# Performance work log

Measured on AMD Instinct MI355X. Metric: run time of the kernel, lower is better.

## Reference

```python
import jax, jax.numpy as jnp
import numpy as np

B, S, D, O, E = 8, 4096, 1024, 1024, 64

def setup_inputs() -> dict:
    key = jax.random.key(0)
    kx, kgw, kgb, kew, keb = jax.random.split(key, 5)
    x = jax.random.normal(kx, (B, S, D), dtype=jnp.float32)
    gate_w = jax.random.normal(kgw, (E, D), dtype=jnp.float32) * 0.02
    gate_b = jnp.zeros((E,), dtype=jnp.float32)
    expert_w = jax.random.normal(kew, (E, D, O), dtype=jnp.float32) * 0.02
    expert_b = jnp.zeros((E, O), dtype=jnp.float32)
    return {"x": x, "gate_w": gate_w, "gate_b": gate_b,
            "expert_w": expert_w, "expert_b": expert_b}

def reference(x, gate_w, gate_b, expert_w, expert_b):
    # x: [B,S,D] -> flatten tokens. With world_size=1 the all-reduce and
    # all-to-alls in the torch module are identities, and per-chunk processing
    # is token-independent, so one global pass is mathematically identical.
    b, s, d = x.shape
    xt = x.reshape(-1, d)                                   # [N, D]
    logits = xt @ gate_w.T + gate_b                         # [N, E]
    gates = jax.nn.softmax(logits, axis=-1)
    sel = jnp.argmax(gates, axis=-1)                        # [N] top-1 expert
    order = jnp.argsort(sel)                                # stable sort by expert
    xs = xt[order]                                          # tokens grouped by expert
    counts = jnp.bincount(sel, length=E).astype(jnp.int32)  # tokens per expert
    # Grouped expert GEMM: row block e of xs multiplies expert_w[e].
    ys = jax.lax.ragged_dot(xs, expert_w, counts)           # [N, O]
    ys = ys + expert_b[sel[order]]
    # Combine: scatter sorted outputs back to original token positions.
    # (Note: torch output is NOT scaled by gate probability.)
    out = jnp.zeros((xt.shape[0], expert_w.shape[-1]), dtype=ys.dtype)
    out = out.at[order].set(ys)
    return out.reshape(b, s, -1)
```

## Files before the change

### kernel.cpp

```cpp
#include <hip/hip_runtime.h>
#include <hip/hip_bf16.h>

#define N_TOK 32768
#define DIM 1024
#define OUTD 1024
#define NEXP 64

typedef __attribute__((ext_vector_type(4))) float f32x4;
typedef __attribute__((ext_vector_type(8))) short bf16x8;

__device__ __forceinline__ unsigned short f2bf(float f) {
    unsigned int u = __builtin_bit_cast(unsigned int, f);
    u += 0x7FFFu + ((u >> 16) & 1u);
    return (unsigned short)(u >> 16);
}

__device__ __forceinline__ uint4 pack8(float4 a, float4 b) {
    uint4 p;
    p.x = (unsigned int)f2bf(a.x) | ((unsigned int)f2bf(a.y) << 16);
    p.y = (unsigned int)f2bf(a.z) | ((unsigned int)f2bf(a.w) << 16);
    p.z = (unsigned int)f2bf(b.x) | ((unsigned int)f2bf(b.y) << 16);
    p.w = (unsigned int)f2bf(b.z) | ((unsigned int)f2bf(b.w) << 16);
    return p;
}

__device__ __forceinline__ float4 ntload4(const float* p) {
    f32x4 v = __builtin_nontemporal_load(reinterpret_cast<const f32x4*>(p));
    float4 r; r.x = v[0]; r.y = v[1]; r.z = v[2]; r.w = v[3];
    return r;
}

#define GLOAD16(gp, lp) \
    __builtin_amdgcn_global_load_lds((const __attribute__((address_space(1))) void*)(gp), \
                                     (__attribute__((address_space(3))) void*)(lp), 16, 0, 0)

__global__ __launch_bounds__(256) void prep_kernel(const float* __restrict__ x,
        const float* __restrict__ gw, const float* __restrict__ gb,
        const float* __restrict__ ew,
        int* __restrict__ sel, int* __restrict__ nflag, int* __restrict__ flags,
        int* __restrict__ counts,
        unsigned short* __restrict__ xb, unsigned short* __restrict__ wt)
{
    __shared__ __align__(16) char smem[18688];
    int tid = threadIdx.x;

    if (blockIdx.x < 512) {
        unsigned short* Ag = (unsigned short*)smem;
        unsigned short* Bg = (unsigned short*)(smem + 8192);
        int* h = (int*)(smem + 16384);
        if (tid < NEXP) h[tid] = 0;

        int t0 = blockIdx.x * 64;
        int lane = tid & 63;
        int w = tid >> 6;
        int lr = lane & 15, lg = lane >> 4;

        int rowS = tid >> 2;
        int koffS = (((tid & 3) ^ ((tid >> 3) & 3)) * 8);
        const float* xsrc = x + (size_t)(t0 + rowS) * DIM + koffS;
        const float* wsrc = gw + (size_t)rowS * DIM + koffS;
        unsigned short* xdst = xb ? xb + (size_t)(t0 + rowS) * DIM + koffS : nullptr;

        f32x4 acc[4];
#pragma unroll
        for (int n = 0; n < 4; n++)
#pragma unroll
            for (int c = 0; c < 4; c++) acc[n][c] = 0.f;

        float4 v0 = *reinterpret_cast<const float4*>(xsrc);
        float4 v1 = *reinterpret_cast<const float4*>(xsrc + 4);
        float4 v2 = *reinterpret_cast<const float4*>(wsrc);
        float4 v3 = *reinterpret_cast<const float4*>(wsrc + 4);
        {
            uint4 pa = pack8(v0, v1), pb = pack8(v2, v3);
            *reinterpret_cast<uint4*>(&Ag[tid * 8]) = pa;
            *reinterpret_cast<uint4*>(&Bg[tid * 8]) = pb;
            if (xdst) *reinterpret_cast<uint4*>(xdst) = pa;
        }
        __syncthreads();

        const char* Agc = (const char*)Ag;
        const char* Bgc = (const char*)Bg;
        int fko = (lg ^ ((lr >> 1) & 3)) * 16;

#pragma unroll 1
        for (int t = 0; t < 32; ++t) {
            if (t < 31) {
                int k0 = (t + 1) * 32;
                v0 = *reinterpret_cast<const float4*>(xsrc + k0);
                v1 = *reinterpret_cast<const float4*>(xsrc + k0 + 4);
                v2 = *reinterpret_cast<const float4*>(wsrc + k0);
                v3 = *reinterpret_cast<const float4*>(wsrc + k0 + 4);
            }
            int boff = (t & 1) * 4096;
            bf16x8 afr = *reinterpret_cast<const bf16x8*>(Agc + boff + ((w * 16 + lr) << 6) + fko);
#pragma unroll
            for (int n = 0; n < 4; n++) {
                bf16x8 bfr = *reinterpret_cast<const bf16x8*>(Bgc + boff + ((n * 16 + lr) << 6) + fko);
                acc[n] = __builtin_amdgcn_mfma_f32_16x16x32_bf16(afr, bfr, acc[n], 0, 0, 0);
            }
            if (t < 31) {
                uint4 pa = pack8(v0, v1), pb = pack8(v2, v3);
                int soff = ((t + 1) & 1) * 2048;
                *reinterpret_cast<uint4*>(&Ag[soff + tid * 8]) = pa;
                *reinterpret_cast<uint4*>(&Bg[soff + tid * 8]) = pb;
                if (xdst) *reinterpret_cast<uint4*>(xdst + (t + 1) * 32) = pa;
            }
            __syncthreads();
        }

        float gbv[4];
#pragma unroll
        for (int n = 0; n < 4; n++) gbv[n] = gb[n * 16 + lr];
#pragma unroll
        for (int i = 0; i < 4; i++) {
            float m1 = -1e30f, m2 = -1e30f; int e1 = 0;
#pragma unroll
            for (int n = 0; n < 4; n++) {
                float v = acc[n][i] + gbv[n];
                if (v > m1) { m2 = m1; m1 = v; e1 = n * 16 + lr; }
                else if (v > m2) m2 = v;
            }
#pragma unroll
            for (int d = 1; d < 16; d <<= 1) {
                float om1 = __shfl_xor(m1, d, 16);
                float om2 = __shfl_xor(m2, d, 16);
                int   oe1 = __shfl_xor(e1, d, 16);
                if (om1 > m1 || (om1 == m1 && oe1 < e1)) {
                    m2 = fmaxf(om2, m1); m1 = om1; e1 = oe1;
                } else {
                    m2 = fmaxf(m2, om1);
                }
            }
            if (lr == 0) {
                int t = t0 + w * 16 + lg * 4 + i;
                sel[t] = e1;
                atomicAdd(&h[e1], 1);
                if (m1 - m2 < 0.01f) {
                    int idx = atomicAdd(nflag, 1);
                    if (idx < 16384) flags[idx] = t;
                }
            }
        }
        __syncthreads();
        if (tid < NEXP && h[tid]) atomicAdd(&counts[tid], h[tid]);
    } else {
        if (!wt) return;
        unsigned short* ts0 = (unsigned short*)smem;
        unsigned short* ts1 = (unsigned short*)(smem + 9216);
        int lin = blockIdx.x - 512;
        int e = lin >> 5;
        int d0 = ((lin >> 4) & 1) * 512;
        int o0 = (lin & 15) * 64;
        const float* src = ew + (size_t)e * (DIM * OUTD);
        unsigned short* dst = wt + (size_t)e * (DIM * OUTD);
        int og = tid & 7;
        int dl = tid >> 3;
        int dc = tid & 7;
        int ol = tid >> 3;

        float4 c0, c1, c2, c3;
        {
            const float* sr0 = &src[(size_t)(d0 + dl) * OUTD + o0 + og * 8];
            const float* sr1 = &src[(size_t)(d0 + dl + 32) * OUTD + o0 + og * 8];
            c0 = ntload4(sr0);
            c1 = ntload4(sr0 + 4);
            c2 = ntload4(sr1);
            c3 = ntload4(sr1 + 4);
        }
#pragma unroll
        for (int s = 0; s < 8; ++s) {
            float4 n0 = c0, n1 = c1, n2 = c2, n3 = c3;
            if (s < 7) {
                int dsn = d0 + (s + 1) * 64;
                const float* sr0 = &src[(size_t)(dsn + dl) * OUTD + o0 + og * 8];
                const float* sr1 = &src[(size_t)(dsn + dl + 32) * OUTD + o0 + og * 8];
                n0 = ntload4(sr0);
                n1 = ntload4(sr0 + 4);
                n2 = ntload4(sr1);
                n3 = ntload4(sr1 + 4);
            }
            unsigned short* tsb = (s & 1) ? ts1 : ts0;
#pragma unroll
            for (int half = 0; half < 2; ++half) {
                int dLoc = dl + 32 * half;
                float4 va = half ? c2 : c0;
                float4 vb = half ? c3 : c1;
                unsigned short b[8] = { f2bf(va.x), f2bf(va.y), f2bf(va.z), f2bf(va.w),
                                        f2bf(vb.x), f2bf(vb.y), f2bf(vb.z), f2bf(vb.w) };
                int dg = dLoc >> 3, dr = dLoc & 7;
#pragma unroll
                for (int k = 0; k < 8; k++) {
                    int o = og * 8 + k;
                    int key = (o & 7) ^ ((o >> 3) & 7);
                    tsb[o * 72 + ((dg ^ key) << 3) + dr] = b[k];
                }
            }
            __syncthreads();
            int ds0 = d0 + s * 64;
#pragma unroll
            for (int i = 0; i < 2; i++) {
                int o = ol + 32 * i;
                int key = (o & 7) ^ ((o >> 3) & 7);
                uint4 v = *reinterpret_cast<const uint4*>(&tsb[o * 72 + ((dc ^ key) << 3)]);
                *reinterpret_cast<uint4*>(&dst[(size_t)(o0 + o) * DIM + ds0 + dc * 8]) = v;
            }
            c0 = n0; c1 = n1; c2 = n2; c3 = n3;
        }
    }
}

__global__ __launch_bounds__(256) void gate_fix_kernel(const float* __restrict__ x,
        const float* __restrict__ gw, const float* __restrict__ gb,
        int* __restrict__ sel, const int* __restrict__ nflag, const int* __restrict__ flags,
        int* __restrict__ counts)
{
    int n = *nflag; if (n > 16384) n = 16384;
    int fi = blockIdx.x * 4 + (threadIdx.x >> 6);
    if (fi >= n) return;
    int t = flags[fi];
    int e = threadIdx.x & 63;
    const float* xr = x + (size_t)t * DIM;
    const float* wr = gw + (size_t)e * DIM;
    double acc = (double)gb[e];
    for (int k = 0; k < DIM; k += 4) {
        acc += (double)xr[k]   * (double)wr[k];
        acc += (double)xr[k+1] * (double)wr[k+1];
        acc += (double)xr[k+2] * (double)wr[k+2];
        acc += (double)xr[k+3] * (double)wr[k+3];
    }
    double m1 = acc; int e1 = e;
#pragma unroll
    for (int d = 1; d < 64; d <<= 1) {
        double om1 = __shfl_xor(m1, d, 64);
        int   oe1  = __shfl_xor(e1, d, 64);
        if (om1 > m1 || (om1 == m1 && oe1 < e1)) { m1 = om1; e1 = oe1; }
    }
    if (e == 0) {
        int eOld = sel[t];
        if (eOld != e1) {
            sel[t] = e1;
            atomicSub(&counts[eOld], 1);
            atomicAdd(&counts[e1], 1);
        }
    }
}

__global__ void sched_kernel(const int* __restrict__ counts, int* __restrict__ offsets,
                             int* __restrict__ schedE, int* __restrict__ schedR,
                             int* __restrict__ totalRB, int rowsShift)
{
    int e = threadIdx.x;
    int c = counts[e];
    int v = c;
#pragma unroll
    for (int d = 1; d < 64; d <<= 1) { int y = __shfl_up(v, d, 64); if (e >= d) v += y; }
    offsets[e] = v - c;
    if (e == 63) offsets[NEXP] = v;
    int rows = 1 << rowsShift;
    int nb = (c + rows - 1) >> rowsShift;
    int rbv = nb;
#pragma unroll
    for (int d = 1; d < 64; d <<= 1) { int y = __shfl_up(rbv, d, 64); if (e >= d) rbv += y; }
    int rbBase = rbv - nb;
    for (int i = 0; i < nb; i++) { schedE[rbBase + i] = e; schedR[rbBase + i] = i << rowsShift; }
    if (e == 63) *totalRB = rbv;
}

__global__ __launch_bounds__(256) void scatter_kernel(const int* __restrict__ sel,
        const int* __restrict__ offsets, int* __restrict__ cursor, int* __restrict__ perm)
{
    int t = blockIdx.x * 256 + threadIdx.x;
    int e = sel[t];
    int pos = offsets[e] + atomicAdd(&cursor[e], 1);
    perm[pos] = t;
}

__global__ __launch_bounds__(512, 4) void moe_gemm7(
        const unsigned short* __restrict__ xb, const unsigned short* __restrict__ wt,
        const float* __restrict__ eb,
        const int* __restrict__ perm, const int* __restrict__ offsets,
        const int* __restrict__ counts, const int* __restrict__ schedE,
        const int* __restrict__ schedR, const int* __restrict__ totalRB,
        float* __restrict__ out)
{
    int idx = blockIdx.x;
    int xcd = idx & 7;
    int s = idx >> 3;
    int cb = s & 7;
    int rb = (s >> 3) * 8 + xcd;
    if (rb >= *totalRB) return;
    int e = schedE[rb], r0 = schedR[rb];
    int cnt = counts[e], base = offsets[e];

    __shared__ __align__(16) unsigned short As[24576];
    __shared__ __align__(16) unsigned short Bs[12288];

    int tid = threadIdx.x;
    int lane = tid & 63;
    int wv = tid >> 6;
    int wr = wv >> 1, wc = wv & 1;
    int lr = lane & 15, lg = lane >> 4;

    int rowS = tid >> 2;
    int koff = ((tid & 3) ^ ((tid >> 3) & 3)) * 8;
    int rA1 = r0 + rowS, rA2 = r0 + 128 + rowS;
    int tokA1 = (rA1 < cnt) ? perm[base + rA1] : 0;
    int tokA2 = (rA2 < cnt) ? perm[base + rA2] : 0;

    const unsigned short* wte = wt + ((size_t)e << 20);
    const unsigned short* aSrc1 = xb + (size_t)tokA1 * DIM + koff;
    const unsigned short* aSrc2 = xb + (size_t)tokA2 * DIM + koff;
    const unsigned short* bSrc1 = wte + (size_t)(cb * 128 + rowS) * DIM + koff;

    unsigned short* AsQ0 = As + wv * 512;
    unsigned short* AsQ1 = As + 4096 + wv * 512;
    unsigned short* BsQ0 = Bs + wv * 512;

    f32x4 acc[4][4];
#pragma unroll
    for (int m = 0; m < 4; m++)
#pragma unroll
        for (int n = 0; n < 4; n++)
#pragma unroll
            for (int c = 0; c < 4; c++) acc[m][n][c] = 0.f;

    const char* Asc = (const char*)As;
    const char* Bsc = (const char*)Bs;
    int fko = (lg ^ ((lr >> 1) & 3)) * 16;

    auto stage = [&](int buf, int k0) {
        GLOAD16(aSrc1 + k0, AsQ0 + buf * 8192);
        GLOAD16(aSrc2 + k0, AsQ1 + buf * 8192);
        GLOAD16(bSrc1 + k0, BsQ0 + buf * 4096);
    };
    auto compute = [&](int buf) {
        int aoff = buf * 16384;
        int boff = buf * 8192;
        bf16x8 bfr[4];
#pragma unroll
        for (int n = 0; n < 4; n++) {
            int row = wc * 64 + n * 16 + lr;
            bfr[n] = *reinterpret_cast<const bf16x8*>(Bsc + boff + (row << 6) + fko);
        }
        __builtin_amdgcn_s_setprio(1);
#pragma unroll
        for (int m = 0; m < 4; m++) {
            int row = wr * 64 + m * 16 + lr;
            bf16x8 afr = *reinterpret_cast<const bf16x8*>(Asc + aoff + (row << 6) + fko);
#pragma unroll
            for (int n = 0; n < 4; n++)
                acc[m][n] = __builtin_amdgcn_mfma_f32_16x16x32_bf16(afr, bfr[n], acc[m][n], 0, 0, 0);
        }
        __builtin_amdgcn_s_setprio(0);
    };

    stage(0, 0);
    stage(1, 32);

    int cbuf = 0, sbuf = 2;
#pragma unroll 1
    for (int t = 0; t < 30; ++t) {
        asm volatile("s_waitcnt vmcnt(3)" ::: "memory");
        __builtin_amdgcn_s_barrier();
        stage(sbuf, (t + 2) * 32);
        compute(cbuf);
        cbuf = (cbuf == 2) ? 0 : cbuf + 1;
        sbuf = (sbuf == 2) ? 0 : sbuf + 1;
    }
    asm volatile("s_waitcnt vmcnt(3)" ::: "memory");
    __builtin_amdgcn_s_barrier();
    compute(cbuf);
    cbuf = (cbuf == 2) ? 0 : cbuf + 1;
    asm volatile("s_waitcnt vmcnt(0)" ::: "memory");
    __builtin_amdgcn_s_barrier();
    compute(cbuf);

    float bias[4];
#pragma unroll
    for (int n = 0; n < 4; n++)
        bias[n] = eb[e * OUTD + cb * 128 + wc * 64 + n * 16 + lr];
#pragma unroll
    for (int m = 0; m < 4; m++) {
        int rowLoc = wr * 64 + m * 16 + lg * 4;
#pragma unroll
        for (int i2 = 0; i2 < 4; i2++) {
            int r = r0 + rowLoc + i2;
            if (r < cnt) {
                int tk = perm[base + r];
                float* op = out + (size_t)tk * OUTD + cb * 128 + wc * 64 + lr;
#pragma unroll
                for (int n = 0; n < 4; n++)
                    __builtin_nontemporal_store(acc[m][n][i2] + bias[n], op + n * 16);
            }
        }
    }
}

extern "C" void kernel_launch(void* const* d_in, const int* in_sizes, int n_in,
                              void* d_out, int out_size, void* d_ws, size_t ws_size,
                              hipStream_t stream)
{
    const float* x  = (const float*)d_in[0];
    const float* gw = (const float*)d_in[1];
    const float* gb = (const float*)d_in[2];
    const float* ew = (const float*)d_in[3];
    const float* eb = (const float*)d_in[4];
    float* out = (float*)d_out;

    char* ws = (char*)d_ws;
    int* counts  = (int*)(ws + 0);
    int* cursor  = (int*)(ws + 256);
    int* offsets = (int*)(ws + 512);
    int* totalRB = (int*)(ws + 1024);
    int* nflag   = (int*)(ws + 1028);
    int* schedE  = (int*)(ws + 2048);
    int* schedR  = (int*)(ws + 4096);
    int* flags   = (int*)(ws + 8192);
    int* sel     = (int*)(ws + 131072);
    int* perm    = (int*)(ws + 262144);

    const size_t WT_OFF   = (size_t)1 << 20;
    const size_t WT_BYTES = (size_t)NEXP * DIM * OUTD * 2;
    const size_t XB_OFF   = WT_OFF + WT_BYTES;
    const size_t XB_BYTES = (size_t)N_TOK * DIM * 2;
    int mode = (ws_size >= XB_OFF + XB_BYTES) ? 2 : 0;
    unsigned short* wt = (mode == 2) ? (unsigned short*)(ws + WT_OFF) : nullptr;
    unsigned short* xb = (mode == 2) ? (unsigned short*)(ws + XB_OFF) : nullptr;

    hipMemsetAsync(ws, 0, 2048, stream);

    prep_kernel<<<dim3(512 + ((mode == 2) ? 2048 : 0)), 256, 0, stream>>>(
        x, gw, gb, ew, sel, nflag, flags, counts, xb, wt);
    gate_fix_kernel<<<dim3(4096), 256, 0, stream>>>(x, gw, gb, sel, nflag, flags, counts);
    sched_kernel<<<dim3(1), 64, 0, stream>>>(counts, offsets, schedE, schedR, totalRB, 8);
    scatter_kernel<<<dim3(N_TOK / 256), 256, 0, stream>>>(sel, offsets, cursor, perm);

    moe_gemm7<<<dim3(1536), 512, 0, stream>>>(xb, wt, eb, perm, offsets, counts,
                                              schedE, schedR, totalRB, out);
}
```

Measured before the change: 379.2 us.

## Fuse gate fix, schedule and scatter into one last-block-ticket kernel

```diff
diff --git a/kernel.cpp b/kernel.cpp
--- a/kernel.cpp
+++ b/kernel.cpp
@@ -210,70 +210,91 @@
     }
 }
 
-__global__ __launch_bounds__(256) void gate_fix_kernel(const float* __restrict__ x,
-        const float* __restrict__ gw, const float* __restrict__ gb,
-        int* __restrict__ sel, const int* __restrict__ nflag, const int* __restrict__ flags,
-        int* __restrict__ counts)
+__global__ __launch_bounds__(256) void fix_sched_scatter_kernel(
+        const float* __restrict__ x, const float* __restrict__ gw,
+        const float* __restrict__ gb, int* __restrict__ sel,
+        const int* __restrict__ nflag, const int* __restrict__ flags,
+        int* __restrict__ counts, int* __restrict__ offsets,
+        int* __restrict__ schedE, int* __restrict__ schedR,
+        int* __restrict__ totalRB, int* __restrict__ ticket,
+        int* __restrict__ perm)
 {
+    __shared__ int amLast;
+    __shared__ int offL[NEXP];
+    __shared__ int curL[NEXP];
+    int tid = threadIdx.x;
+    int wv = tid >> 6, lane = tid & 63;
     int n = *nflag; if (n > 16384) n = 16384;
-    int fi = blockIdx.x * 4 + (threadIdx.x >> 6);
-    if (fi >= n) return;
-    int t = flags[fi];
-    int e = threadIdx.x & 63;
-    const float* xr = x + (size_t)t * DIM;
-    const float* wr = gw + (size_t)e * DIM;
-    double acc = (double)gb[e];
-    for (int k = 0; k < DIM; k += 4) {
-        acc += (double)xr[k]   * (double)wr[k];
-        acc += (double)xr[k+1] * (double)wr[k+1];
-        acc += (double)xr[k+2] * (double)wr[k+2];
-        acc += (double)xr[k+3] * (double)wr[k+3];
-    }
-    double m1 = acc; int e1 = e;
-#pragma unroll
-    for (int d = 1; d < 64; d <<= 1) {
-        double om1 = __shfl_xor(m1, d, 64);
-        int   oe1  = __shfl_xor(e1, d, 64);
-        if (om1 > m1 || (om1 == m1 && oe1 < e1)) { m1 = om1; e1 = oe1; }
-    }
-    if (e == 0) {
-        int eOld = sel[t];
-        if (eOld != e1) {
-            sel[t] = e1;
-            atomicSub(&counts[eOld], 1);
-            atomicAdd(&counts[e1], 1);
-        }
-    }
-}
-
-__global__ void sched_kernel(const int* __restrict__ counts, int* __restrict__ offsets,
-                             int* __restrict__ schedE, int* __restrict__ schedR,
-                             int* __restrict__ totalRB, int rowsShift)
-{
-    int e = threadIdx.x;
-    int c = counts[e];
-    int v = c;
-#pragma unroll
-    for (int d = 1; d < 64; d <<= 1) { int y = __shfl_up(v, d, 64); if (e >= d) v += y; }
-    offsets[e] = v - c;
-    if (e == 63) offsets[NEXP] = v;
-    int rows = 1 << rowsShift;
-    int nb = (c + rows - 1) >> rowsShift;
-    int rbv = nb;
-#pragma unroll
-    for (int d = 1; d < 64; d <<= 1) { int y = __shfl_up(rbv, d, 64); if (e >= d) rbv += y; }
-    int rbBase = rbv - nb;
-    for (int i = 0; i < nb; i++) { schedE[rbBase + i] = e; schedR[rbBase + i] = i << rowsShift; }
-    if (e == 63) *totalRB = rbv;
-}
-
-__global__ __launch_bounds__(256) void scatter_kernel(const int* __restrict__ sel,
-        const int* __restrict__ offsets, int* __restrict__ cursor, int* __restrict__ perm)
-{
-    int t = blockIdx.x * 256 + threadIdx.x;
-    int e = sel[t];
-    int pos = offsets[e] + atomicAdd(&cursor[e], 1);
-    perm[pos] = t;
+
+    for (int j = 0; j < 4; ++j) {
+        int fi = blockIdx.x * 16 + wv * 4 + j;
+        if (fi >= n) break;
+        int t = flags[fi];
+        const float* xr = x + (size_t)t * DIM;
+        const float* wr = gw + (size_t)lane * DIM;
+        double a0 = 0, a1 = 0, a2 = 0, a3 = 0;
+        for (int k = 0; k < DIM; k += 8) {
+            a0 += (double)xr[k]     * (double)wr[k];
+            a1 += (double)xr[k + 1] * (double)wr[k + 1];
+            a2 += (double)xr[k + 2] * (double)wr[k + 2];
+            a3 += (double)xr[k + 3] * (double)wr[k + 3];
+            a0 += (double)xr[k + 4] * (double)wr[k + 4];
+            a1 += (double)xr[k + 5] * (double)wr[k + 5];
+            a2 += (double)xr[k + 6] * (double)wr[k + 6];
+            a3 += (double)xr[k + 7] * (double)wr[k + 7];
+        }
+        double m1 = ((a0 + a1) + (a2 + a3)) + (double)gb[lane];
+        int e1 = lane;
+#pragma unroll
+        for (int d = 1; d < 64; d <<= 1) {
+            double om1 = __shfl_xor(m1, d, 64);
+            int   oe1  = __shfl_xor(e1, d, 64);
+            if (om1 > m1 || (om1 == m1 && oe1 < e1)) { m1 = om1; e1 = oe1; }
+        }
+        if (lane == 0) {
+            int eOld = sel[t];
+            if (eOld != e1) {
+                sel[t] = e1;
+                atomicSub(&counts[eOld], 1);
+                atomicAdd(&counts[e1], 1);
+            }
+        }
+    }
+
+    __threadfence();
+    __syncthreads();
+    if (tid == 0)
+        amLast = (atomicAdd(ticket, 1) == (int)gridDim.x - 1);
+    __syncthreads();
+    if (!amLast) return;
+    __threadfence();
+
+    if (wv == 0) {
+        int c = counts[lane];
+        int v = c;
+#pragma unroll
+        for (int d = 1; d < 64; d <<= 1) { int y = __shfl_up(v, d, 64); if (lane >= d) v += y; }
+        offsets[lane] = v - c;
+        offL[lane] = v - c;
+        curL[lane] = 0;
+        if (lane == 63) offsets[NEXP] = v;
+        int nb = (c + 255) >> 8;
+        int rbv = nb;
+#pragma unroll
+        for (int d = 1; d < 64; d <<= 1) { int y = __shfl_up(rbv, d, 64); if (lane >= d) rbv += y; }
+        int rbBase = rbv - nb;
+        for (int i = 0; i < nb; i++) { schedE[rbBase + i] = lane; schedR[rbBase + i] = i << 8; }
+        if (lane == 63) *totalRB = rbv;
+    }
+    __syncthreads();
+
+#pragma unroll 8
+    for (int it = 0; it < N_TOK / 256; ++it) {
+        int t = it * 256 + tid;
+        int e = sel[t];
+        int pos = offL[e] + atomicAdd(&curL[e], 1);
+        perm[pos] = t;
+    }
 }
 
 __global__ __launch_bounds__(512, 4) void moe_gemm7(
@@ -410,10 +431,10 @@
 
     char* ws = (char*)d_ws;
     int* counts  = (int*)(ws + 0);
-    int* cursor  = (int*)(ws + 256);
     int* offsets = (int*)(ws + 512);
     int* totalRB = (int*)(ws + 1024);
     int* nflag   = (int*)(ws + 1028);
+    int* ticket  = (int*)(ws + 1036);
     int* schedE  = (int*)(ws + 2048);
     int* schedR  = (int*)(ws + 4096);
     int* flags   = (int*)(ws + 8192);
@@ -432,10 +453,9 @@
 
     prep_kernel<<<dim3(512 + ((mode == 2) ? 2048 : 0)), 256, 0, stream>>>(
         x, gw, gb, ew, sel, nflag, flags, counts, xb, wt);
-    gate_fix_kernel<<<dim3(4096), 256, 0, stream>>>(x, gw, gb, sel, nflag, flags, counts);
-    sched_kernel<<<dim3(1), 64, 0, stream>>>(counts, offsets, schedE, schedR, totalRB, 8);
-    scatter_kernel<<<dim3(N_TOK / 256), 256, 0, stream>>>(sel, offsets, cursor, perm);
-
+    fix_sched_scatter_kernel<<<dim3(1024), 256, 0, stream>>>(
+        x, gw, gb, sel, nflag, flags, counts, offsets, schedE, schedR,
+        totalRB, ticket, perm);
     moe_gemm7<<<dim3(1536), 512, 0, stream>>>(xb, wt, eb, perm, offsets, counts,
                                               schedE, schedR, totalRB, out);
 }
```

Result: slower. 483.5 us (+27.5%).
